# Performance work log

Hardware: AMD Instinct MI355X
Metric: run time of the kernel (lower is better)

The kernel has to match this reference:

```python
import jax, jax.numpy as jnp
import numpy as np

D_MODEL = 1024
N_HEADS = 16
HEAD_DIM = D_MODEL // N_HEADS


def setup_inputs() -> dict:
    key = jax.random.key(0)
    ks = jax.random.split(key, 5)
    s = 1.0 / np.sqrt(D_MODEL)
    return {
        "x": jax.random.normal(ks[0], (2, 2048, D_MODEL), dtype=jnp.float32),
        "w_qkv": jax.random.uniform(ks[1], (3 * D_MODEL, D_MODEL), jnp.float32, -s, s),
        "b_qkv": jax.random.uniform(ks[2], (3 * D_MODEL,), jnp.float32, -s, s),
        "w_out": jax.random.uniform(ks[3], (D_MODEL, D_MODEL), jnp.float32, -s, s),
        "b_out": jax.random.uniform(ks[4], (D_MODEL,), jnp.float32, -s, s),
    }


def _attn(x, w_qkv, b_qkv, w_out, b_out):
    bsz, seq_len, _ = x.shape
    qkv = jnp.einsum('bsd,ed->bse', x, w_qkv) + b_qkv  # [B,S,3D]
    q, k, v = jnp.split(qkv, 3, axis=-1)
    def heads(t):  # [B,S,D] -> [B,H,S,Dh]
        return t.reshape(bsz, seq_len, N_HEADS, HEAD_DIM).transpose(0, 2, 1, 3)
    q, k, v = heads(q), heads(k), heads(v)
    scores = jnp.einsum('bhqd,bhkd->bhqk', q, k) / np.sqrt(HEAD_DIM)
    mask = jnp.tril(jnp.ones((seq_len, seq_len), dtype=bool))
    scores = jnp.where(mask, scores, -jnp.inf)
    probs = jax.nn.softmax(scores, axis=-1)
    attn = jnp.einsum('bhqk,bhkd->bhqd', probs, v)
    attn = attn.transpose(0, 2, 1, 3).reshape(bsz, seq_len, D_MODEL)
    return jnp.einsum('bsd,ed->bse', attn, w_out) + b_out


def reference(x, w_qkv, b_qkv, w_out, b_out):
    return _attn(x, w_qkv, b_qkv, w_out, b_out)
```

## Files before the change

### kernel.cpp

```cpp
#include <hip/hip_runtime.h>
#include <hip/hip_bf16.h>
#include <stdint.h>

#define SEQ     2048
#define BATCH   2
#define NHEADS  16
#define HDIM    64
#define DMODEL  1024
#define N3      3072
#define D2      2048
#define MTOT    (BATCH*SEQ)

typedef __attribute__((ext_vector_type(4))) float f32x4;
typedef __attribute__((ext_vector_type(8))) short bf16x8;

static __device__ inline unsigned short f2bf(float f) {
    union { float f; unsigned u; } v; v.f = f;
    unsigned r = (v.u + 0x7fffu + ((v.u >> 16) & 1u)) >> 16;
    return (unsigned short)r;
}
static __device__ inline unsigned pk2bf(float a, float b) {
    union { __hip_bfloat162 h; unsigned u; } c;
    c.h = __float22bfloat162_rn(make_float2(a, b));
    return c.u;
}

#define GLDS(gp, lp) __builtin_amdgcn_global_load_lds( \
    (const __attribute__((address_space(1))) void*)(gp), \
    (__attribute__((address_space(3))) void*)(lp), 16, 0, 0)

__global__ void cast_all(const float* __restrict__ x,
                         const float* __restrict__ wqkv,
                         const float* __restrict__ wout,
                         unsigned short* __restrict__ xb,
                         unsigned short* __restrict__ wqkvb,
                         unsigned short* __restrict__ woutb) {
    long i4 = (long)(blockIdx.x * blockDim.x + threadIdx.x) * 4;
    const float* src; unsigned short* dst; long off;
    if (i4 < 4194304L)      { src = x;    dst = xb;    off = i4; }
    else if (i4 < 7340032L) { src = wqkv; dst = wqkvb; off = i4 - 4194304L; }
    else                    { src = wout; dst = woutb; off = i4 - 7340032L; }
    float4 v = *(const float4*)(src + off);
    union { uint2 u; ushort4 s; } pk;
    pk.u.x = pk2bf(v.x, v.y); pk.u.y = pk2bf(v.z, v.w);
    *(ushort4*)(dst + off) = pk.s;
}

__global__ __launch_bounds__(256, 2) void gemm_qkv(
    const unsigned short* __restrict__ A,
    const unsigned short* __restrict__ B,
    const float* __restrict__ bias,
    unsigned short* __restrict__ qk,
    unsigned short* __restrict__ vT)
{
    __shared__ __align__(16) unsigned short sA[2][128][64];
    __shared__ __align__(16) unsigned short sB[2][128][64];
    const int tid  = threadIdx.x;
    const int wave = tid >> 6, lane = tid & 63;
    const int quad = lane >> 4, l16 = lane & 15, l7 = l16 & 7;
    const int wm = wave >> 1, wn = wave & 1;
    const int m0 = blockIdx.x * 128, n0 = blockIdx.y * 128;

    f32x4 acc[4][4];
    const f32x4 zero = {0.f, 0.f, 0.f, 0.f};
    #pragma unroll
    for (int i = 0; i < 4; i++)
        #pragma unroll
        for (int j = 0; j < 4; j++) acc[i][j] = zero;

    const int rsel = tid >> 3;
    const int sgl  = (tid & 7) ^ (rsel & 7);
    const unsigned short* gA0 = A + (long)(m0 + rsel) * 1024 + sgl * 8;
    const unsigned short* gB0 = B + (long)(n0 + rsel) * 1024 + sgl * 8;

    #pragma unroll
    for (int i = 0; i < 4; i++) {
        GLDS(gA0 + (long)(32 * i) * 1024, &sA[0][32 * i + wave * 8][0]);
        GLDS(gB0 + (long)(32 * i) * 1024, &sB[0][32 * i + wave * 8][0]);
    }

    int buf = 0;
    for (int k0 = 0; k0 < 1024; k0 += 64, buf ^= 1) {
        __syncthreads();
        if (k0 + 64 < 1024) {
            #pragma unroll
            for (int i = 0; i < 4; i++) {
                GLDS(gA0 + (long)(32 * i) * 1024 + k0 + 64, &sA[buf ^ 1][32 * i + wave * 8][0]);
                GLDS(gB0 + (long)(32 * i) * 1024 + k0 + 64, &sB[buf ^ 1][32 * i + wave * 8][0]);
            }
        }
        #pragma unroll
        for (int ks = 0; ks < 2; ks++) {
            bf16x8 af[4], bfr[4];
            #pragma unroll
            for (int mt = 0; mt < 4; mt++)
                af[mt] = *(const bf16x8*)(&sA[buf][wm * 64 + mt * 16 + l16][((ks * 4 + quad) ^ l7) * 8]);
            #pragma unroll
            for (int nt = 0; nt < 4; nt++)
                bfr[nt] = *(const bf16x8*)(&sB[buf][wn * 64 + nt * 16 + l16][((ks * 4 + quad) ^ l7) * 8]);
            #pragma unroll
            for (int mt = 0; mt < 4; mt++)
                #pragma unroll
                for (int nt = 0; nt < 4; nt++)
                    acc[mt][nt] = __builtin_amdgcn_mfma_f32_16x16x32_bf16(
                        af[mt], bfr[nt], acc[mt][nt], 0, 0, 0);
        }
    }

    if (n0 < 2048) {
        #pragma unroll
        for (int nt = 0; nt < 4; nt++) {
            const int n_g = n0 + wn * 64 + nt * 16 + l16;
            const float bv = bias[n_g];
            #pragma unroll
            for (int mt = 0; mt < 4; mt++) {
                #pragma unroll
                for (int r = 0; r < 4; r++) {
                    const int m_g = m0 + wm * 64 + mt * 16 + quad * 4 + r;
                    qk[(long)m_g * D2 + n_g] = f2bf(acc[mt][nt][r] + bv);
                }
            }
        }
    } else {
        const int b = m0 >> 11;
        #pragma unroll
        for (int nt = 0; nt < 4; nt++) {
            const int n_g = n0 + wn * 64 + nt * 16 + l16;
            const int dm = n_g - 2048;
            const long vrow = (long)(((b << 4) + (dm >> 6)) << 6) + (dm & 63);
            const float bv = bias[n_g];
            #pragma unroll
            for (int mt = 0; mt < 4; mt++) {
                const int m_g = m0 + wm * 64 + mt * 16 + quad * 4;
                union { uint2 u; ushort4 s; } pk;
                pk.u.x = pk2bf(acc[mt][nt][0] + bv, acc[mt][nt][1] + bv);
                pk.u.y = pk2bf(acc[mt][nt][2] + bv, acc[mt][nt][3] + bv);
                *(ushort4*)(vT + vrow * D2 + (m_g & 2047)) = pk.s;
            }
        }
    }
}

__global__ __launch_bounds__(256, 2) void gemm_out(
    const unsigned short* __restrict__ A,
    const unsigned short* __restrict__ B,
    const float* __restrict__ bias,
    float* __restrict__ C)
{
    __shared__ __align__(16) unsigned short sA[2][128][64];
    __shared__ __align__(16) unsigned short sB[2][64][64];
    const int tid  = threadIdx.x;
    const int wave = tid >> 6, lane = tid & 63;
    const int quad = lane >> 4, l16 = lane & 15, l7 = l16 & 7;
    const int wm = wave >> 1, wn = wave & 1;
    const int m0 = blockIdx.x * 128, n0 = blockIdx.y * 64;

    f32x4 acc[4][2];
    const f32x4 zero = {0.f, 0.f, 0.f, 0.f};
    #pragma unroll
    for (int i = 0; i < 4; i++) { acc[i][0] = zero; acc[i][1] = zero; }

    const int rsel = tid >> 3;
    const int sgl  = (tid & 7) ^ (rsel & 7);
    const unsigned short* gA0 = A + (long)(m0 + rsel) * 1024 + sgl * 8;
    const unsigned short* gB0 = B + (long)(n0 + rsel) * 1024 + sgl * 8;

    #pragma unroll
    for (int i = 0; i < 4; i++)
        GLDS(gA0 + (long)(32 * i) * 1024, &sA[0][32 * i + wave * 8][0]);
    #pragma unroll
    for (int i = 0; i < 2; i++)
        GLDS(gB0 + (long)(32 * i) * 1024, &sB[0][32 * i + wave * 8][0]);

    int buf = 0;
    for (int k0 = 0; k0 < 1024; k0 += 64, buf ^= 1) {
        __syncthreads();
        if (k0 + 64 < 1024) {
            #pragma unroll
            for (int i = 0; i < 4; i++)
                GLDS(gA0 + (long)(32 * i) * 1024 + k0 + 64, &sA[buf ^ 1][32 * i + wave * 8][0]);
            #pragma unroll
            for (int i = 0; i < 2; i++)
                GLDS(gB0 + (long)(32 * i) * 1024 + k0 + 64, &sB[buf ^ 1][32 * i + wave * 8][0]);
        }
        #pragma unroll
        for (int ks = 0; ks < 2; ks++) {
            bf16x8 af[4], bfr[2];
            #pragma unroll
            for (int mt = 0; mt < 4; mt++)
                af[mt] = *(const bf16x8*)(&sA[buf][wm * 64 + mt * 16 + l16][((ks * 4 + quad) ^ l7) * 8]);
            #pragma unroll
            for (int nt = 0; nt < 2; nt++)
                bfr[nt] = *(const bf16x8*)(&sB[buf][wn * 32 + nt * 16 + l16][((ks * 4 + quad) ^ l7) * 8]);
            #pragma unroll
            for (int mt = 0; mt < 4; mt++)
                #pragma unroll
                for (int nt = 0; nt < 2; nt++)
                    acc[mt][nt] = __builtin_amdgcn_mfma_f32_16x16x32_bf16(
                        af[mt], bfr[nt], acc[mt][nt], 0, 0, 0);
        }
    }
    #pragma unroll
    for (int nt = 0; nt < 2; nt++) {
        const int n_g = n0 + wn * 32 + nt * 16 + l16;
        const float bv = bias[n_g];
        #pragma unroll
        for (int mt = 0; mt < 4; mt++) {
            #pragma unroll
            for (int r = 0; r < 4; r++) {
                const int m_g = m0 + wm * 64 + mt * 16 + quad * 4 + r;
                C[(long)m_g * DMODEL + n_g] = acc[mt][nt][r] + bv;
            }
        }
    }
}

__global__ __launch_bounds__(256, 2) void attn_kernel(
    const unsigned short* __restrict__ qk,
    const unsigned short* __restrict__ vT,
    unsigned short* __restrict__ attn)
{
    __shared__ __align__(16) unsigned short sK [2][2][64][64];
    __shared__ __align__(16) unsigned short sVt[2][2][64][64];
    __shared__ __align__(16) unsigned short sP [4][16][64];

    const int tid  = threadIdx.x;
    const int w    = tid >> 6, lane = tid & 63;
    const int quad = lane >> 4, l16 = lane & 15, l7 = l16 & 7;

    const int bh = blockIdx.x;
    const int b  = bh >> 4, h = bh & 15;
    const int pair = blockIdx.y;
    const long rowb = (long)b * SEQ;

    const int rl = lane >> 3;
    const int sm = (lane & 7) ^ rl;
    const unsigned short* kg = qk + (rowb + w * 16 + rl) * D2 + 1024 + h * HDIM + sm * 8;
    const unsigned short* vg = vT + (long)(bh * 64 + w * 16 + rl) * D2 + sm * 8;

    const int s0 = quad ^ l7;
    const float C2 = 0.18033688011112042f;
    const f32x4 zero = {0.f, 0.f, 0.f, 0.f};

    #pragma unroll
    for (int ph = 0; ph < 2; ph++) {
        const int qtile  = ph ? (31 - pair) : pair;
        const int qbase  = qtile * 64;
        const int ntiles = qtile + 1;
        const int npairs = (ntiles + 1) >> 1;

        bf16x8 qf0, qf1;
        {
            const unsigned short* qp = qk + (rowb + qbase + w * 16 + l16) * D2 + h * HDIM;
            qf0 = *(const bf16x8*)(qp + quad * 8);
            qf1 = *(const bf16x8*)(qp + 32 + quad * 8);
        }
        f32x4 Oacc[4];
        #pragma unroll
        for (int mf = 0; mf < 4; mf++) Oacc[mf] = zero;
        float l_i = 0.f;

        __syncthreads();
        {
            const long o0 = 0, o1 = (long)(1 <= qtile ? 1 : qtile) * 64;
            GLDS(kg + o0 * D2,           &sK [0][0][w * 16][0]);
            GLDS(kg + o0 * D2 + 8L * D2, &sK [0][0][w * 16 + 8][0]);
            GLDS(vg + o0,                &sVt[0][0][w * 16][0]);
            GLDS(vg + o0 + 8L * D2,      &sVt[0][0][w * 16 + 8][0]);
            GLDS(kg + o1 * D2,           &sK [0][1][w * 16][0]);
            GLDS(kg + o1 * D2 + 8L * D2, &sK [0][1][w * 16 + 8][0]);
            GLDS(vg + o1,                &sVt[0][1][w * 16][0]);
            GLDS(vg + o1 + 8L * D2,      &sVt[0][1][w * 16 + 8][0]);
        }

        int buf = 0;
        for (int p = 0; p < npairs; p++, buf ^= 1) {
            __syncthreads();
            if (p + 1 < npairs) {
                const int t0 = 2 * p + 2, t1 = 2 * p + 3;
                const long o0 = (long)(t0 <= qtile ? t0 : qtile) * 64;
                const long o1 = (long)(t1 <= qtile ? t1 : qtile) * 64;
                GLDS(kg + o0 * D2,           &sK [buf ^ 1][0][w * 16][0]);
                GLDS(kg + o0 * D2 + 8L * D2, &sK [buf ^ 1][0][w * 16 + 8][0]);
                GLDS(vg + o0,                &sVt[buf ^ 1][0][w * 16][0]);
                GLDS(vg + o0 + 8L * D2,      &sVt[buf ^ 1][0][w * 16 + 8][0]);
                GLDS(kg + o1 * D2,           &sK [buf ^ 1][1][w * 16][0]);
                GLDS(kg + o1 * D2 + 8L * D2, &sK [buf ^ 1][1][w * 16 + 8][0]);
                GLDS(vg + o1,                &sVt[buf ^ 1][1][w * 16][0]);
                GLDS(vg + o1 + 8L * D2,      &sVt[buf ^ 1][1][w * 16 + 8][0]);
            }
            #pragma unroll
            for (int s = 0; s < 2; s++) {
                const int t = 2 * p + s;
                if (t >= ntiles) break;

                f32x4 st[4];
                #pragma unroll
                for (int kvf = 0; kvf < 4; kvf++) {
                    bf16x8 kf0 = *(const bf16x8*)(&sK[buf][s][kvf * 16 + l16][s0 * 8]);
                    bf16x8 kf1 = *(const bf16x8*)(&sK[buf][s][kvf * 16 + l16][(s0 ^ 4) * 8]);
                    st[kvf] = __builtin_amdgcn_mfma_f32_16x16x32_bf16(kf0, qf0, zero, 0, 0, 0);
                    st[kvf] = __builtin_amdgcn_mfma_f32_16x16x32_bf16(kf1, qf1, st[kvf], 0, 0, 0);
                }
                if (t == qtile) {
                    const int ql = w * 16 + l16;
                    #pragma unroll
                    for (int kvf = 0; kvf < 4; kvf++) {
                        const int kv = kvf * 16 + quad * 4;
                        #pragma unroll
                        for (int r = 0; r < 4; r++)
                            if (kv + r > ql) st[kvf][r] = -1e30f;
                    }
                }
                #pragma unroll
                for (int kvf = 0; kvf < 4; kvf++) {
                    #pragma unroll
                    for (int r = 0; r < 4; r++)
                        st[kvf][r] = __builtin_amdgcn_exp2f(st[kvf][r] * C2);
                }
                f32x4 ps = (st[0] + st[1]) + (st[2] + st[3]);
                l_i += (ps[0] + ps[1]) + (ps[2] + ps[3]);

                #pragma unroll
                for (int kvf = 0; kvf < 4; kvf++) {
                    union { uint2 u; ushort4 s4; } pk;
                    pk.u.x = pk2bf(st[kvf][0], st[kvf][1]);
                    pk.u.y = pk2bf(st[kvf][2], st[kvf][3]);
                    const int seg = (kvf * 2 + (quad >> 1)) ^ l7;
                    *(ushort4*)(&sP[w][l16][seg * 8 + (quad & 1) * 4]) = pk.s4;
                }
                bf16x8 pf0 = *(const bf16x8*)(&sP[w][l16][(quad ^ l7) * 8]);
                bf16x8 pf1 = *(const bf16x8*)(&sP[w][l16][((4 + quad) ^ l7) * 8]);
                #pragma unroll
                for (int mf = 0; mf < 4; mf++) {
                    bf16x8 vf0 = *(const bf16x8*)(&sVt[buf][s][mf * 16 + l16][s0 * 8]);
                    bf16x8 vf1 = *(const bf16x8*)(&sVt[buf][s][mf * 16 + l16][(s0 ^ 4) * 8]);
                    Oacc[mf] = __builtin_amdgcn_mfma_f32_16x16x32_bf16(vf0, pf0, Oacc[mf], 0, 0, 0);
                    Oacc[mf] = __builtin_amdgcn_mfma_f32_16x16x32_bf16(vf1, pf1, Oacc[mf], 0, 0, 0);
                }
            }
        }
        float L = l_i;
        L += __shfl_xor(L, 16);
        L += __shfl_xor(L, 32);
        const float inv = 1.0f / L;
        const int q = qbase + w * 16 + l16;
        unsigned short* op = attn + (rowb + q) * DMODEL + h * HDIM + quad * 4;
        #pragma unroll
        for (int mf = 0; mf < 4; mf++) {
            union { uint2 u; ushort4 s4; } pk;
            pk.u.x = pk2bf(Oacc[mf][0] * inv, Oacc[mf][1] * inv);
            pk.u.y = pk2bf(Oacc[mf][2] * inv, Oacc[mf][3] * inv);
            *(ushort4*)(op + mf * 16) = pk.s4;
        }
    }
}

extern "C" void kernel_launch(void* const* d_in, const int* in_sizes, int n_in,
                              void* d_out, int out_size, void* d_ws, size_t ws_size,
                              hipStream_t stream) {
    const float* x    = (const float*)d_in[0];
    const float* wqkv = (const float*)d_in[1];
    const float* bqkv = (const float*)d_in[2];
    const float* wout = (const float*)d_in[3];
    const float* bout = (const float*)d_in[4];

    char* ws = (char*)d_ws;
    unsigned short* xb    = (unsigned short*)(ws);
    unsigned short* wqkvb = (unsigned short*)(ws + (8L << 20));
    unsigned short* woutb = (unsigned short*)(ws + (14L << 20));
    unsigned short* qkb   = (unsigned short*)(ws + (16L << 20));
    unsigned short* vTb   = (unsigned short*)(ws + (32L << 20));
    unsigned short* attnb = (unsigned short*)(ws + (40L << 20));

    cast_all<<<8192, 256, 0, stream>>>(x, wqkv, wout, xb, wqkvb, woutb);

    dim3 g1(32, 24);
    gemm_qkv<<<g1, 256, 0, stream>>>(xb, wqkvb, bqkv, qkb, vTb);

    dim3 g2(32, 16);
    attn_kernel<<<g2, 256, 0, stream>>>(qkb, vTb, attnb);

    dim3 g3(32, 16);
    gemm_out<<<g3, 256, 0, stream>>>(attnb, woutb, bout, (float*)d_out);
}
```

Baseline: 175.5 us.

## Retile QKV GEMM to 128x192, shrink out-GEMM K-tile, and give attention waves 32 query rows

The QKV GEMM moves to 128x192 output tiles, giving 512 blocks instead of 768, and now handles blocks whose columns span both the QK and V regions. The output GEMM halves its K-tile to 32, which cuts LDS use so the launch bound can rise to 4 blocks per SM. The attention kernel drops to 2 waves per block, each covering 32 query rows, so every K/V fragment loaded from LDS feeds twice as many MFMAs. Each change trades occupancy or register pressure against more data reuse and fewer blocks.

```diff
diff --git a/kernel.cpp b/kernel.cpp
--- a/kernel.cpp
+++ b/kernel.cpp
@@ -54,19 +54,19 @@
     unsigned short* __restrict__ vT)
 {
     __shared__ __align__(16) unsigned short sA[2][128][64];
-    __shared__ __align__(16) unsigned short sB[2][128][64];
+    __shared__ __align__(16) unsigned short sB[2][192][64];
     const int tid  = threadIdx.x;
     const int wave = tid >> 6, lane = tid & 63;
     const int quad = lane >> 4, l16 = lane & 15, l7 = l16 & 7;
     const int wm = wave >> 1, wn = wave & 1;
-    const int m0 = blockIdx.x * 128, n0 = blockIdx.y * 128;
-
-    f32x4 acc[4][4];
+    const int m0 = blockIdx.x * 128, n0 = blockIdx.y * 192;
+
+    f32x4 acc[4][6];
     const f32x4 zero = {0.f, 0.f, 0.f, 0.f};
     #pragma unroll
     for (int i = 0; i < 4; i++)
         #pragma unroll
-        for (int j = 0; j < 4; j++) acc[i][j] = zero;
+        for (int j = 0; j < 6; j++) acc[i][j] = zero;
 
     const int rsel = tid >> 3;
     const int sgl  = (tid & 7) ^ (rsel & 7);
@@ -74,44 +74,48 @@
     const unsigned short* gB0 = B + (long)(n0 + rsel) * 1024 + sgl * 8;
 
     #pragma unroll
-    for (int i = 0; i < 4; i++) {
+    for (int i = 0; i < 4; i++)
         GLDS(gA0 + (long)(32 * i) * 1024, &sA[0][32 * i + wave * 8][0]);
+    #pragma unroll
+    for (int i = 0; i < 6; i++)
         GLDS(gB0 + (long)(32 * i) * 1024, &sB[0][32 * i + wave * 8][0]);
-    }
 
     int buf = 0;
     for (int k0 = 0; k0 < 1024; k0 += 64, buf ^= 1) {
         __syncthreads();
         if (k0 + 64 < 1024) {
             #pragma unroll
-            for (int i = 0; i < 4; i++) {
+            for (int i = 0; i < 4; i++)
                 GLDS(gA0 + (long)(32 * i) * 1024 + k0 + 64, &sA[buf ^ 1][32 * i + wave * 8][0]);
+            #pragma unroll
+            for (int i = 0; i < 6; i++)
                 GLDS(gB0 + (long)(32 * i) * 1024 + k0 + 64, &sB[buf ^ 1][32 * i + wave * 8][0]);
-            }
         }
         #pragma unroll
         for (int ks = 0; ks < 2; ks++) {
-            bf16x8 af[4], bfr[4];
+            const int fseg = ((ks * 4 + quad) ^ l7) * 8;
+            bf16x8 af[4], bfr[6];
             #pragma unroll
             for (int mt = 0; mt < 4; mt++)
-                af[mt] = *(const bf16x8*)(&sA[buf][wm * 64 + mt * 16 + l16][((ks * 4 + quad) ^ l7) * 8]);
-            #pragma unroll
-            for (int nt = 0; nt < 4; nt++)
-                bfr[nt] = *(const bf16x8*)(&sB[buf][wn * 64 + nt * 16 + l16][((ks * 4 + quad) ^ l7) * 8]);
+                af[mt] = *(const bf16x8*)(&sA[buf][wm * 64 + mt * 16 + l16][fseg]);
+            #pragma unroll
+            for (int nt = 0; nt < 6; nt++)
+                bfr[nt] = *(const bf16x8*)(&sB[buf][wn * 96 + nt * 16 + l16][fseg]);
             #pragma unroll
             for (int mt = 0; mt < 4; mt++)
                 #pragma unroll
-                for (int nt = 0; nt < 4; nt++)
+                for (int nt = 0; nt < 6; nt++)
                     acc[mt][nt] = __builtin_amdgcn_mfma_f32_16x16x32_bf16(
                         af[mt], bfr[nt], acc[mt][nt], 0, 0, 0);
         }
     }
 
-    if (n0 < 2048) {
-        #pragma unroll
-        for (int nt = 0; nt < 4; nt++) {
-            const int n_g = n0 + wn * 64 + nt * 16 + l16;
-            const float bv = bias[n_g];
+    const int b = m0 >> 11;
+    #pragma unroll
+    for (int nt = 0; nt < 6; nt++) {
+        const int n_g = n0 + wn * 96 + nt * 16 + l16;
+        const float bv = bias[n_g];
+        if (n_g < 2048) {
             #pragma unroll
             for (int mt = 0; mt < 4; mt++) {
                 #pragma unroll
@@ -120,15 +124,9 @@
                     qk[(long)m_g * D2 + n_g] = f2bf(acc[mt][nt][r] + bv);
                 }
             }
-        }
-    } else {
-        const int b = m0 >> 11;
-        #pragma unroll
-        for (int nt = 0; nt < 4; nt++) {
-            const int n_g = n0 + wn * 64 + nt * 16 + l16;
+        } else {
             const int dm = n_g - 2048;
             const long vrow = (long)(((b << 4) + (dm >> 6)) << 6) + (dm & 63);
-            const float bv = bias[n_g];
             #pragma unroll
             for (int mt = 0; mt < 4; mt++) {
                 const int m_g = m0 + wm * 64 + mt * 16 + quad * 4;
@@ -141,17 +139,17 @@
     }
 }
 
-__global__ __launch_bounds__(256, 2) void gemm_out(
+__global__ __launch_bounds__(256, 4) void gemm_out(
     const unsigned short* __restrict__ A,
     const unsigned short* __restrict__ B,
     const float* __restrict__ bias,
     float* __restrict__ C)
 {
-    __shared__ __align__(16) unsigned short sA[2][128][64];
-    __shared__ __align__(16) unsigned short sB[2][64][64];
+    __shared__ __align__(16) unsigned short sA[2][128][32];
+    __shared__ __align__(16) unsigned short sB[2][64][32];
     const int tid  = threadIdx.x;
     const int wave = tid >> 6, lane = tid & 63;
-    const int quad = lane >> 4, l16 = lane & 15, l7 = l16 & 7;
+    const int quad = lane >> 4, l16 = lane & 15;
     const int wm = wave >> 1, wn = wave & 1;
     const int m0 = blockIdx.x * 128, n0 = blockIdx.y * 64;
 
@@ -160,45 +158,38 @@
     #pragma unroll
     for (int i = 0; i < 4; i++) { acc[i][0] = zero; acc[i][1] = zero; }
 
-    const int rsel = tid >> 3;
-    const int sgl  = (tid & 7) ^ (rsel & 7);
+    const int rsel = tid >> 2;
+    const int sgl  = (tid & 3) ^ ((tid >> 3) & 3);
     const unsigned short* gA0 = A + (long)(m0 + rsel) * 1024 + sgl * 8;
     const unsigned short* gB0 = B + (long)(n0 + rsel) * 1024 + sgl * 8;
 
-    #pragma unroll
-    for (int i = 0; i < 4; i++)
-        GLDS(gA0 + (long)(32 * i) * 1024, &sA[0][32 * i + wave * 8][0]);
-    #pragma unroll
-    for (int i = 0; i < 2; i++)
-        GLDS(gB0 + (long)(32 * i) * 1024, &sB[0][32 * i + wave * 8][0]);
+    const int fs = (quad ^ ((l16 >> 1) & 3)) * 8;
+
+    GLDS(gA0,              &sA[0][wave * 16][0]);
+    GLDS(gA0 + 64L * 1024, &sA[0][64 + wave * 16][0]);
+    GLDS(gB0,              &sB[0][wave * 16][0]);
 
     int buf = 0;
-    for (int k0 = 0; k0 < 1024; k0 += 64, buf ^= 1) {
+    for (int k0 = 0; k0 < 1024; k0 += 32, buf ^= 1) {
         __syncthreads();
-        if (k0 + 64 < 1024) {
-            #pragma unroll
-            for (int i = 0; i < 4; i++)
-                GLDS(gA0 + (long)(32 * i) * 1024 + k0 + 64, &sA[buf ^ 1][32 * i + wave * 8][0]);
-            #pragma unroll
-            for (int i = 0; i < 2; i++)
-                GLDS(gB0 + (long)(32 * i) * 1024 + k0 + 64, &sB[buf ^ 1][32 * i + wave * 8][0]);
-        }
-        #pragma unroll
-        for (int ks = 0; ks < 2; ks++) {
-            bf16x8 af[4], bfr[2];
-            #pragma unroll
-            for (int mt = 0; mt < 4; mt++)
-                af[mt] = *(const bf16x8*)(&sA[buf][wm * 64 + mt * 16 + l16][((ks * 4 + quad) ^ l7) * 8]);
+        if (k0 + 32 < 1024) {
+            GLDS(gA0 + k0 + 32,              &sA[buf ^ 1][wave * 16][0]);
+            GLDS(gA0 + 64L * 1024 + k0 + 32, &sA[buf ^ 1][64 + wave * 16][0]);
+            GLDS(gB0 + k0 + 32,              &sB[buf ^ 1][wave * 16][0]);
+        }
+        bf16x8 af[4], bfr[2];
+        #pragma unroll
+        for (int mt = 0; mt < 4; mt++)
+            af[mt] = *(const bf16x8*)(&sA[buf][wm * 64 + mt * 16 + l16][fs]);
+        #pragma unroll
+        for (int nt = 0; nt < 2; nt++)
+            bfr[nt] = *(const bf16x8*)(&sB[buf][wn * 32 + nt * 16 + l16][fs]);
+        #pragma unroll
+        for (int mt = 0; mt < 4; mt++)
             #pragma unroll
             for (int nt = 0; nt < 2; nt++)
-                bfr[nt] = *(const bf16x8*)(&sB[buf][wn * 32 + nt * 16 + l16][((ks * 4 + quad) ^ l7) * 8]);
-            #pragma unroll
-            for (int mt = 0; mt < 4; mt++)
-                #pragma unroll
-                for (int nt = 0; nt < 2; nt++)
-                    acc[mt][nt] = __builtin_amdgcn_mfma_f32_16x16x32_bf16(
-                        af[mt], bfr[nt], acc[mt][nt], 0, 0, 0);
-        }
+                acc[mt][nt] = __builtin_amdgcn_mfma_f32_16x16x32_bf16(
+                    af[mt], bfr[nt], acc[mt][nt], 0, 0, 0);
     }
     #pragma unroll
     for (int nt = 0; nt < 2; nt++) {
@@ -215,14 +206,14 @@
     }
 }
 
-__global__ __launch_bounds__(256, 2) void attn_kernel(
+__global__ __launch_bounds__(128) void attn_kernel(
     const unsigned short* __restrict__ qk,
     const unsigned short* __restrict__ vT,
     unsigned short* __restrict__ attn)
 {
     __shared__ __align__(16) unsigned short sK [2][2][64][64];
     __shared__ __align__(16) unsigned short sVt[2][2][64][64];
-    __shared__ __align__(16) unsigned short sP [4][16][64];
+    __shared__ __align__(16) unsigned short sP [2][2][16][64];
 
     const int tid  = threadIdx.x;
     const int w    = tid >> 6, lane = tid & 63;
@@ -235,8 +226,8 @@
 
     const int rl = lane >> 3;
     const int sm = (lane & 7) ^ rl;
-    const unsigned short* kg = qk + (rowb + w * 16 + rl) * D2 + 1024 + h * HDIM + sm * 8;
-    const unsigned short* vg = vT + (long)(bh * 64 + w * 16 + rl) * D2 + sm * 8;
+    const unsigned short* kg = qk + (rowb + w * 32 + rl) * D2 + 1024 + h * HDIM + sm * 8;
+    const unsigned short* vg = vT + (long)(bh * 64 + w * 32 + rl) * D2 + sm * 8;
 
     const int s0 = quad ^ l7;
     const float C2 = 0.18033688011112042f;
@@ -249,28 +240,28 @@
         const int ntiles = qtile + 1;
         const int npairs = (ntiles + 1) >> 1;
 
-        bf16x8 qf0, qf1;
-        {
-            const unsigned short* qp = qk + (rowb + qbase + w * 16 + l16) * D2 + h * HDIM;
-            qf0 = *(const bf16x8*)(qp + quad * 8);
-            qf1 = *(const bf16x8*)(qp + 32 + quad * 8);
-        }
-        f32x4 Oacc[4];
-        #pragma unroll
-        for (int mf = 0; mf < 4; mf++) Oacc[mf] = zero;
-        float l_i = 0.f;
+        bf16x8 qfr[2][2];
+        #pragma unroll
+        for (int qf = 0; qf < 2; qf++) {
+            const unsigned short* qp = qk + (rowb + qbase + w * 32 + qf * 16 + l16) * D2 + h * HDIM;
+            qfr[qf][0] = *(const bf16x8*)(qp + quad * 8);
+            qfr[qf][1] = *(const bf16x8*)(qp + 32 + quad * 8);
+        }
+        f32x4 Oacc[4][2];
+        #pragma unroll
+        for (int mf = 0; mf < 4; mf++) { Oacc[mf][0] = zero; Oacc[mf][1] = zero; }
+        float l_i[2] = {0.f, 0.f};
 
         __syncthreads();
         {
-            const long o0 = 0, o1 = (long)(1 <= qtile ? 1 : qtile) * 64;
-            GLDS(kg + o0 * D2,           &sK [0][0][w * 16][0]);
-            GLDS(kg + o0 * D2 + 8L * D2, &sK [0][0][w * 16 + 8][0]);
-            GLDS(vg + o0,                &sVt[0][0][w * 16][0]);
-            GLDS(vg + o0 + 8L * D2,      &sVt[0][0][w * 16 + 8][0]);
-            GLDS(kg + o1 * D2,           &sK [0][1][w * 16][0]);
-            GLDS(kg + o1 * D2 + 8L * D2, &sK [0][1][w * 16 + 8][0]);
-            GLDS(vg + o1,                &sVt[0][1][w * 16][0]);
-            GLDS(vg + o1 + 8L * D2,      &sVt[0][1][w * 16 + 8][0]);
+            const int o0 = 0, o1 = (1 <= qtile ? 1 : qtile) * 64;
+            #pragma unroll
+            for (int i = 0; i < 4; i++) {
+                GLDS(kg + (long)(o0 + 8 * i) * D2, &sK [0][0][w * 32 + 8 * i][0]);
+                GLDS(vg + o0 + (long)(8 * i) * D2, &sVt[0][0][w * 32 + 8 * i][0]);
+                GLDS(kg + (long)(o1 + 8 * i) * D2, &sK [0][1][w * 32 + 8 * i][0]);
+                GLDS(vg + o1 + (long)(8 * i) * D2, &sVt[0][1][w * 32 + 8 * i][0]);
+            }
         }
 
         int buf = 0;
@@ -278,80 +269,97 @@
             __syncthreads();
             if (p + 1 < npairs) {
                 const int t0 = 2 * p + 2, t1 = 2 * p + 3;
-                const long o0 = (long)(t0 <= qtile ? t0 : qtile) * 64;
-                const long o1 = (long)(t1 <= qtile ? t1 : qtile) * 64;
-                GLDS(kg + o0 * D2,           &sK [buf ^ 1][0][w * 16][0]);
-                GLDS(kg + o0 * D2 + 8L * D2, &sK [buf ^ 1][0][w * 16 + 8][0]);
-                GLDS(vg + o0,                &sVt[buf ^ 1][0][w * 16][0]);
-                GLDS(vg + o0 + 8L * D2,      &sVt[buf ^ 1][0][w * 16 + 8][0]);
-                GLDS(kg + o1 * D2,           &sK [buf ^ 1][1][w * 16][0]);
-                GLDS(kg + o1 * D2 + 8L * D2, &sK [buf ^ 1][1][w * 16 + 8][0]);
-                GLDS(vg + o1,                &sVt[buf ^ 1][1][w * 16][0]);
-                GLDS(vg + o1 + 8L * D2,      &sVt[buf ^ 1][1][w * 16 + 8][0]);
+                const int o0 = (t0 <= qtile ? t0 : qtile) * 64;
+                const int o1 = (t1 <= qtile ? t1 : qtile) * 64;
+                #pragma unroll
+                for (int i = 0; i < 4; i++) {
+                    GLDS(kg + (long)(o0 + 8 * i) * D2, &sK [buf ^ 1][0][w * 32 + 8 * i][0]);
+                    GLDS(vg + o0 + (long)(8 * i) * D2, &sVt[buf ^ 1][0][w * 32 + 8 * i][0]);
+                    GLDS(kg + (long)(o1 + 8 * i) * D2, &sK [buf ^ 1][1][w * 32 + 8 * i][0]);
+                    GLDS(vg + o1 + (long)(8 * i) * D2, &sVt[buf ^ 1][1][w * 32 + 8 * i][0]);
+                }
             }
             #pragma unroll
             for (int s = 0; s < 2; s++) {
                 const int t = 2 * p + s;
                 if (t >= ntiles) break;
 
-                f32x4 st[4];
+                f32x4 st[4][2];
                 #pragma unroll
                 for (int kvf = 0; kvf < 4; kvf++) {
                     bf16x8 kf0 = *(const bf16x8*)(&sK[buf][s][kvf * 16 + l16][s0 * 8]);
                     bf16x8 kf1 = *(const bf16x8*)(&sK[buf][s][kvf * 16 + l16][(s0 ^ 4) * 8]);
-                    st[kvf] = __builtin_amdgcn_mfma_f32_16x16x32_bf16(kf0, qf0, zero, 0, 0, 0);
-                    st[kvf] = __builtin_amdgcn_mfma_f32_16x16x32_bf16(kf1, qf1, st[kvf], 0, 0, 0);
+                    #pragma unroll
+                    for (int qf = 0; qf < 2; qf++) {
+                        st[kvf][qf] = __builtin_amdgcn_mfma_f32_16x16x32_bf16(kf0, qfr[qf][0], zero, 0, 0, 0);
+                        st[kvf][qf] = __builtin_amdgcn_mfma_f32_16x16x32_bf16(kf1, qfr[qf][1], st[kvf][qf], 0, 0, 0);
+                    }
                 }
                 if (t == qtile) {
-                    const int ql = w * 16 + l16;
+                    #pragma unroll
+                    for (int qf = 0; qf < 2; qf++) {
+                        const int ql = w * 32 + qf * 16 + l16;
+                        #pragma unroll
+                        for (int kvf = 0; kvf < 4; kvf++) {
+                            const int kv = kvf * 16 + quad * 4;
+                            #pragma unroll
+                            for (int r = 0; r < 4; r++)
+                                if (kv + r > ql) st[kvf][qf][r] = -1e30f;
+                        }
+                    }
+                }
+                #pragma unroll
+                for (int qf = 0; qf < 2; qf++) {
                     #pragma unroll
                     for (int kvf = 0; kvf < 4; kvf++) {
-                        const int kv = kvf * 16 + quad * 4;
                         #pragma unroll
                         for (int r = 0; r < 4; r++)
-                            if (kv + r > ql) st[kvf][r] = -1e30f;
-                    }
-                }
-                #pragma unroll
-                for (int kvf = 0; kvf < 4; kvf++) {
-                    #pragma unroll
-                    for (int r = 0; r < 4; r++)
-                        st[kvf][r] = __builtin_amdgcn_exp2f(st[kvf][r] * C2);
-                }
-                f32x4 ps = (st[0] + st[1]) + (st[2] + st[3]);
-                l_i += (ps[0] + ps[1]) + (ps[2] + ps[3]);
-
-                #pragma unroll
-                for (int kvf = 0; kvf < 4; kvf++) {
-                    union { uint2 u; ushort4 s4; } pk;
-                    pk.u.x = pk2bf(st[kvf][0], st[kvf][1]);
-                    pk.u.y = pk2bf(st[kvf][2], st[kvf][3]);
-                    const int seg = (kvf * 2 + (quad >> 1)) ^ l7;
-                    *(ushort4*)(&sP[w][l16][seg * 8 + (quad & 1) * 4]) = pk.s4;
-                }
-                bf16x8 pf0 = *(const bf16x8*)(&sP[w][l16][(quad ^ l7) * 8]);
-                bf16x8 pf1 = *(const bf16x8*)(&sP[w][l16][((4 + quad) ^ l7) * 8]);
+                            st[kvf][qf][r] = __builtin_amdgcn_exp2f(st[kvf][qf][r] * C2);
+                    }
+                    f32x4 ps = (st[0][qf] + st[1][qf]) + (st[2][qf] + st[3][qf]);
+                    l_i[qf] += (ps[0] + ps[1]) + (ps[2] + ps[3]);
+                    #pragma unroll
+                    for (int kvf = 0; kvf < 4; kvf++) {
+                        union { uint2 u; ushort4 s4; } pk;
+                        pk.u.x = pk2bf(st[kvf][qf][0], st[kvf][qf][1]);
+                        pk.u.y = pk2bf(st[kvf][qf][2], st[kvf][qf][3]);
+                        const int seg = (kvf * 2 + (quad >> 1)) ^ l7;
+                        *(ushort4*)(&sP[w][qf][l16][seg * 8 + (quad & 1) * 4]) = pk.s4;
+                    }
+                }
+                bf16x8 pf[2][2];
+                #pragma unroll
+                for (int qf = 0; qf < 2; qf++) {
+                    pf[qf][0] = *(const bf16x8*)(&sP[w][qf][l16][(quad ^ l7) * 8]);
+                    pf[qf][1] = *(const bf16x8*)(&sP[w][qf][l16][((4 + quad) ^ l7) * 8]);
+                }
                 #pragma unroll
                 for (int mf = 0; mf < 4; mf++) {
                     bf16x8 vf0 = *(const bf16x8*)(&sVt[buf][s][mf * 16 + l16][s0 * 8]);
                     bf16x8 vf1 = *(const bf16x8*)(&sVt[buf][s][mf * 16 + l16][(s0 ^ 4) * 8]);
-                    Oacc[mf] = __builtin_amdgcn_mfma_f32_16x16x32_bf16(vf0, pf0, Oacc[mf], 0, 0, 0);
-                    Oacc[mf] = __builtin_amdgcn_mfma_f32_16x16x32_bf16(vf1, pf1, Oacc[mf], 0, 0, 0);
-                }
-            }
-        }
-        float L = l_i;
-        L += __shfl_xor(L, 16);
-        L += __shfl_xor(L, 32);
-        const float inv = 1.0f / L;
-        const int q = qbase + w * 16 + l16;
-        unsigned short* op = attn + (rowb + q) * DMODEL + h * HDIM + quad * 4;
-        #pragma unroll
-        for (int mf = 0; mf < 4; mf++) {
-            union { uint2 u; ushort4 s4; } pk;
-            pk.u.x = pk2bf(Oacc[mf][0] * inv, Oacc[mf][1] * inv);
-            pk.u.y = pk2bf(Oacc[mf][2] * inv, Oacc[mf][3] * inv);
-            *(ushort4*)(op + mf * 16) = pk.s4;
+                    #pragma unroll
+                    for (int qf = 0; qf < 2; qf++) {
+                        Oacc[mf][qf] = __builtin_amdgcn_mfma_f32_16x16x32_bf16(vf0, pf[qf][0], Oacc[mf][qf], 0, 0, 0);
+                        Oacc[mf][qf] = __builtin_amdgcn_mfma_f32_16x16x32_bf16(vf1, pf[qf][1], Oacc[mf][qf], 0, 0, 0);
+                    }
+                }
+            }
+        }
+        #pragma unroll
+        for (int qf = 0; qf < 2; qf++) {
+            float L = l_i[qf];
+            L += __shfl_xor(L, 16);
+            L += __shfl_xor(L, 32);
+            const float inv = 1.0f / L;
+            const int q = qbase + w * 32 + qf * 16 + l16;
+            unsigned short* op = attn + (rowb + q) * DMODEL + h * HDIM + quad * 4;
+            #pragma unroll
+            for (int mf = 0; mf < 4; mf++) {
+                union { uint2 u; ushort4 s4; } pk;
+                pk.u.x = pk2bf(Oacc[mf][qf][0] * inv, Oacc[mf][qf][1] * inv);
+                pk.u.y = pk2bf(Oacc[mf][qf][2] * inv, Oacc[mf][qf][3] * inv);
+                *(ushort4*)(op + mf * 16) = pk.s4;
+            }
         }
     }
 }
@@ -375,11 +383,11 @@
 
     cast_all<<<8192, 256, 0, stream>>>(x, wqkv, wout, xb, wqkvb, woutb);
 
-    dim3 g1(32, 24);
+    dim3 g1(32, 16);
     gemm_qkv<<<g1, 256, 0, stream>>>(xb, wqkvb, bqkv, qkb, vTb);
 
     dim3 g2(32, 16);
-    attn_kernel<<<g2, 256, 0, stream>>>(qkb, vTb, attnb);
+    attn_kernel<<<g2, 128, 0, stream>>>(qkb, vTb, attnb);
 
     dim3 g3(32, 16);
     gemm_out<<<g3, 256, 0, stream>>>(attnb, woutb, bout, (float*)d_out);
```

New measurement: 178.1 us. No clear change (+1.5%).
